# Performance work log

Hardware: AMD Instinct MI355X
Metric: run time of the kernel (lower is better)

## Reference

```python
import jax, jax.numpy as jnp
import numpy as np

# Module config (matches init_kwargs): inp_modes=[16,4,4,4], out_modes=[16,4,4,4], ranks=[1,8,8,1], 3x3 kernel
C_IN0, C_OUT0 = 16, 16          # leading conv channels
INP_MODES = (4, 4, 4)            # TT input modes -> c_inp = 64
OUT_MODES = (4, 4, 4)            # TT output modes -> c_out = 64
RANKS = (1, 8, 8, 1)
C_INP = int(np.prod(INP_MODES))  # 64
C_OUT = int(np.prod(OUT_MODES))  # 64


def setup_inputs() -> dict:
    key = jax.random.key(0)
    ks = jax.random.split(key, 5)
    x = jax.random.normal(ks[0], (8, C_IN0 * C_INP, 64, 64), jnp.float32)
    kernel = jax.random.normal(ks[1], (C_OUT0, C_IN0, 3, 3), jnp.float32) * (2.0 / (C_IN0 + C_OUT0))
    cores = {}
    for k in range(3):
        m, n = INP_MODES[k], OUT_MODES[k]
        cores[f"core{k}"] = jax.random.normal(ks[2 + k], (RANKS[k], m, n, RANKS[k + 1]), jnp.float32) * (2.0 / (m + n))
    b = jnp.ones((C_OUT,), jnp.float32)
    return {"x": x, "kernel": kernel, **cores, "b": b}


def _tt_matrix(core0, core1, core2):
    # Reconstruct W[(i1 i2 i3), (j1 j2 j3)] from TT cores (r_k, m_k, n_k, r_{k+1}).
    Wm = core0[0]  # (m1, n1, r1)  since r0 == 1
    for c in (core1, core2):
        Wm = jnp.einsum('...r,rmns->...mns', Wm, c)  # append (m_k, n_k) modes
    Wm = Wm[..., 0]  # drop trailing rank (== 1): (m1,n1,m2,n2,m3,n3)
    Wm = jnp.transpose(Wm, (0, 2, 4, 1, 3, 5))       # (m1,m2,m3,n1,n2,n3)
    return Wm.reshape(C_INP, C_OUT)


def reference(x, kernel, core0, core1, core2, b):
    B, Cin, H, W = x.shape  # Cin = C_IN0 * C_INP
    xr = x.reshape(-1, C_IN0, H, W)  # (B*c_inp, c_inp_0, H, W)
    y = jax.lax.conv_general_dilated(
        xr, kernel, window_strides=(1, 1), padding='VALID',
        dimension_numbers=('NCHW', 'OIHW', 'NCHW'))  # (B*c_inp, c_out_0, h, w)
    h, w = y.shape[-2], y.shape[-1]
    # Follow the torch reshape chain exactly
    y = y.reshape(B, C_INP, -1)                 # (B, c_inp, c_out_0*h*w)
    y = jnp.transpose(y, (0, 2, 1)).reshape(-1, C_INP)  # (B*c_out_0*h*w, c_inp)
    Wm = _tt_matrix(core0, core1, core2)        # (c_inp, c_out)
    out = y @ Wm + b                             # (B*c_out_0*h*w, c_out)
    return out.reshape(B, C_OUT0 * C_OUT, h, w)
```

## Files before the change

kernel.cpp:

```cpp
#include <hip/hip_runtime.h>
#include <hip/hip_bf16.h>

#define NB    8
#define NG    64
#define NCI   16
#define NC0   16
#define NJ    64
#define IH    64
#define IW    64
#define OH    62
#define OW    62
#define IPIX  4096
#define OPIX  3844

typedef __attribute__((ext_vector_type(8))) short  short8;
typedef __attribute__((ext_vector_type(4))) short  short4v;
typedef __attribute__((ext_vector_type(4))) float  float4v;

__device__ __forceinline__ unsigned short f2bf(float f) {
    unsigned int u = __builtin_bit_cast(unsigned int, f);
    unsigned int r = (u + 0x7fffu + ((u >> 16) & 1u)) >> 16;
    return (unsigned short)r;
}

__global__ __launch_bounds__(64) void prep_kernel(const float* __restrict__ K,
                                                  const float* __restrict__ c0_,
                                                  const float* __restrict__ c1_,
                                                  const float* __restrict__ c2_,
                                                  unsigned short* __restrict__ wmb,
                                                  unsigned short* __restrict__ kb) {
    int bi = blockIdx.x;
    int l  = threadIdx.x;
    if (bi < 8) {
        int jt = bi >> 1, kh = bi & 1;
        int j = jt * 16 + (l & 15);
        int j1 = j >> 4, j2 = (j >> 2) & 3, j3 = j & 3;
        for (int i = 0; i < 8; ++i) {
            int g = kh * 32 + (l >> 4) * 8 + i;
            int i1 = g >> 4, i2 = (g >> 2) & 3, i3 = g & 3;
            float s = 0.f;
            #pragma unroll
            for (int r1 = 0; r1 < 8; ++r1) {
                float a = c0_[(i1 * 4 + j1) * 8 + r1];
                float t = 0.f;
                #pragma unroll
                for (int r2 = 0; r2 < 8; ++r2) {
                    t += c1_[((r1 * 4 + i2) * 4 + j2) * 8 + r2] *
                         c2_[(r2 * 4 + i3) * 4 + j3];
                }
                s += a * t;
            }
            wmb[(bi * 64 + l) * 8 + i] = f2bf(s);
        }
    } else {
        int c0i = l & 15, q = l >> 4;
        for (int f = 0; f < 5; ++f) {
            int tap = f * 2 + (q >> 1);
            for (int i = 0; i < 8; ++i) {
                int ci = (q & 1) * 8 + i;
                float v = (tap < 9) ? K[(c0i * 16 + ci) * 9 + tap] : 0.f;
                kb[(f * 64 + l) * 8 + i] = f2bf(v);
            }
        }
    }
}

__global__ __launch_bounds__(256) void mix2_kernel(const float* __restrict__ x,
                                                   const unsigned short* __restrict__ wmb,
                                                   unsigned short* __restrict__ Z) {
    __shared__ __align__(16) char smem[32 * 2048];
    int t  = threadIdx.x;
    int b  = blockIdx.x >> 7;
    int p0 = (blockIdx.x & 127) * 32;

    int pq  = (t & 7) * 4;
    int grp = t >> 3;
    const float* xb = x + (size_t)b * 1024 * IPIX + p0 + pq;
    #pragma unroll 2
    for (int it = 0; it < 8; ++it) {
        int qd = it * 32 + grp;
        int gq = qd & 15, ci = qd >> 4;
        int g0 = gq * 4;
        const float* xp = xb + (size_t)(g0 * 16 + ci) * IPIX;
        float4v v0 = *(const float4v*)(xp);
        float4v v1 = *(const float4v*)(xp + 16 * IPIX);
        float4v v2 = *(const float4v*)(xp + 32 * IPIX);
        float4v v3 = *(const float4v*)(xp + 48 * IPIX);
        #pragma unroll
        for (int pp = 0; pp < 4; ++pp) {
            int px = pq + pp;
            short4v u;
            u[0] = (short)f2bf(v0[pp]);
            u[1] = (short)f2bf(v1[pp]);
            u[2] = (short)f2bf(v2[pp]);
            u[3] = (short)f2bf(v3[pp]);
            int chunk = (g0 >> 3) ^ (ci & 7) ^ (px & 7);
            *(short4v*)(smem + px * 2048 + ci * 128 + chunk * 16 + (g0 & 7) * 2) = u;
        }
    }
    __syncthreads();

    int lane = t & 63, wv = t >> 6;
    int ln = lane & 15, quad = lane >> 4;

    short8 bf[8];
    #pragma unroll
    for (int q8 = 0; q8 < 8; ++q8)
        bf[q8] = *(const short8*)(wmb + (q8 * 64 + lane) * 8);

    unsigned short* Zb = Z + (size_t)(b * IPIX + p0) * 1024;
    for (int k = 0; k < 8; ++k) {
        int pl = wv * 8 + k;
        const char* arow = smem + pl * 2048 + ln * 128;
        int sw = (ln & 7) ^ (pl & 7);
        short8 a0 = *(const short8*)(arow + (((0 + quad) ^ sw) * 16));
        short8 a1 = *(const short8*)(arow + (((4 + quad) ^ sw) * 16));
        unsigned short* zp = Zb + (size_t)pl * 1024 + ln * 16 + quad * 4;
        #pragma unroll
        for (int jt = 0; jt < 4; ++jt) {
            float4v acc = {0.f, 0.f, 0.f, 0.f};
            acc = __builtin_amdgcn_mfma_f32_16x16x32_bf16(a0, bf[jt * 2 + 0], acc, 0, 0, 0);
            acc = __builtin_amdgcn_mfma_f32_16x16x32_bf16(a1, bf[jt * 2 + 1], acc, 0, 0, 0);
            short4v o;
            o[0] = (short)f2bf(acc[0]); o[1] = (short)f2bf(acc[1]);
            o[2] = (short)f2bf(acc[2]); o[3] = (short)f2bf(acc[3]);
            *(short4v*)(zp + jt * 256) = o;
        }
    }
}

__global__ __launch_bounds__(256, 4) void conv2_kernel(const unsigned short* __restrict__ Z,
                                                       const unsigned short* __restrict__ kb,
                                                       const float* __restrict__ bias,
                                                       float* __restrict__ out) {
    int t = threadIdx.x, lane = t & 63, wv = t >> 6;
    int ln = lane & 15, quad = lane >> 4;
    int blk = blockIdx.x;
    int xh = blk & 1;
    int y  = (blk >> 1) % OH;
    int b  = blk / (OH * 2);

    short8 af[5];
    int off[5];
    #pragma unroll
    for (int f = 0; f < 5; ++f) {
        af[f] = *(const short8*)(kb + (f * 64 + lane) * 8);
        int tap = f * 2 + (quad >> 1);
        if (tap > 8) tap = 8;
        int dy = tap / 3, dx = tap % 3;
        off[f] = (dy * IW + dx) * 1024 + (wv * 16 + ln) * 16 + (quad & 1) * 8;
    }
    float4v bv = *(const float4v*)(bias + wv * 16 + quad * 4);

    const unsigned short* zbase = Z + (size_t)(b * IPIX + y * IW + xh * 31) * 1024;
    float* ob = out + ((size_t)(b * NC0 + ln) * OPIX + (size_t)(y * OW + xh * 31)) * NJ
                    + wv * 16 + quad * 4;

    #pragma unroll 2
    for (int xi = 0; xi < 31; ++xi) {
        const unsigned short* zp = zbase + (size_t)xi * 1024;
        short8 z0 = *(const short8*)(zp + off[0]);
        short8 z1 = *(const short8*)(zp + off[1]);
        short8 z2 = *(const short8*)(zp + off[2]);
        short8 z3 = *(const short8*)(zp + off[3]);
        short8 z4 = *(const short8*)(zp + off[4]);
        float4v acc = bv;
        acc = __builtin_amdgcn_mfma_f32_16x16x32_bf16(z0, af[0], acc, 0, 0, 0);
        acc = __builtin_amdgcn_mfma_f32_16x16x32_bf16(z1, af[1], acc, 0, 0, 0);
        acc = __builtin_amdgcn_mfma_f32_16x16x32_bf16(z2, af[2], acc, 0, 0, 0);
        acc = __builtin_amdgcn_mfma_f32_16x16x32_bf16(z3, af[3], acc, 0, 0, 0);
        acc = __builtin_amdgcn_mfma_f32_16x16x32_bf16(z4, af[4], acc, 0, 0, 0);
        *(float4v*)(ob + (size_t)xi * NJ) = acc;
    }
}

__global__ __launch_bounds__(64) void wm_kernel(const float* __restrict__ core0,
                                                const float* __restrict__ core1,
                                                const float* __restrict__ core2,
                                                float* __restrict__ Wm) {
    int g = threadIdx.x;
    int i1 = g >> 4, i2 = (g >> 2) & 3, i3 = g & 3;
    for (int j = 0; j < NJ; ++j) {
        int j1 = j >> 4, j2 = (j >> 2) & 3, j3 = j & 3;
        float s = 0.f;
        #pragma unroll
        for (int r1 = 0; r1 < 8; ++r1) {
            float a = core0[(i1 * 4 + j1) * 8 + r1];
            float t = 0.f;
            #pragma unroll
            for (int r2 = 0; r2 < 8; ++r2) {
                t += core1[((r1 * 4 + i2) * 4 + j2) * 8 + r2] *
                     core2[(r2 * 4 + i3) * 4 + j3];
            }
            s += a * t;
        }
        Wm[g * NJ + j] = s;
    }
}

__global__ __launch_bounds__(256) void fused_fallback(const float* __restrict__ x,
                                                      const float* __restrict__ K,
                                                      const float* __restrict__ Wm,
                                                      const float* __restrict__ bias,
                                                      float* __restrict__ out) {
    __shared__ float wlds[NG * NJ];
    __shared__ float klds[NCI * 9];
    int blk  = blockIdx.x;
    int pblk = blk & 15;
    int c0   = (blk >> 4) & 15;
    int b    = blk >> 8;
    for (int i = threadIdx.x; i < NG * NJ; i += 256) wlds[i] = Wm[i];
    for (int i = threadIdx.x; i < NCI * 9; i += 256) klds[i] = K[c0 * NCI * 9 + i];
    __syncthreads();

    int pix = pblk * 256 + threadIdx.x;
    if (pix >= OPIX) return;
    int y  = pix / OW;
    int xx = pix % OW;

    float acc[NJ];
    #pragma unroll
    for (int j = 0; j < NJ; ++j) acc[j] = 0.f;

    for (int g = 0; g < NG; ++g) {
        float c = 0.f;
        const float* xb = x + ((size_t)(b * NG + g) * NCI) * IPIX;
        for (int ci = 0; ci < NCI; ++ci) {
            #pragma unroll
            for (int dy = 0; dy < 3; ++dy) {
                #pragma unroll
                for (int dx = 0; dx < 3; ++dx) {
                    c += xb[ci * IPIX + (y + dy) * IW + (xx + dx)] *
                         klds[ci * 9 + dy * 3 + dx];
                }
            }
        }
        const float4* wp = (const float4*)&wlds[g * NJ];
        #pragma unroll
        for (int j4 = 0; j4 < 16; ++j4) {
            float4 w = wp[j4];
            acc[j4 * 4 + 0] += w.x * c;
            acc[j4 * 4 + 1] += w.y * c;
            acc[j4 * 4 + 2] += w.z * c;
            acc[j4 * 4 + 3] += w.w * c;
        }
    }
    #pragma unroll
    for (int j = 0; j < NJ; ++j) {
        out[(((size_t)(b * NC0 + c0) * OPIX) + pix) * NJ + j] = acc[j] + bias[j];
    }
}

extern "C" void kernel_launch(void* const* d_in, const int* in_sizes, int n_in,
                              void* d_out, int out_size, void* d_ws, size_t ws_size,
                              hipStream_t stream) {
    const float* x     = (const float*)d_in[0];
    const float* K     = (const float*)d_in[1];
    const float* core0 = (const float*)d_in[2];
    const float* core1 = (const float*)d_in[3];
    const float* core2 = (const float*)d_in[4];
    const float* bias  = (const float*)d_in[5];
    float* out = (float*)d_out;

    const size_t z_off   = 16384;
    const size_t z_bytes = (size_t)NB * IPIX * NJ * NCI * sizeof(unsigned short);

    if (ws_size >= z_off + z_bytes + 256) {
        unsigned short* wmb = (unsigned short*)d_ws;
        unsigned short* kb  = (unsigned short*)((char*)d_ws + 8192);
        unsigned short* Z   = (unsigned short*)((char*)d_ws + z_off);
        prep_kernel<<<9, 64, 0, stream>>>(K, core0, core1, core2, wmb, kb);
        mix2_kernel<<<NB * 128, 256, 0, stream>>>(x, wmb, Z);
        conv2_kernel<<<NB * OH * 2, 256, 0, stream>>>(Z, kb, bias, out);
    } else {
        float* Wm = (float*)d_ws;
        wm_kernel<<<1, 64, 0, stream>>>(core0, core1, core2, Wm);
        fused_fallback<<<NB * NC0 * 16, 256, 0, stream>>>(x, K, Wm, bias, out);
    }
}
```

Before: 113.4 us.

## Split mixing into separate transpose-to-bf16 pass and LDS-free MFMA mix kernel

Moves the fp32-to-bf16 conversion and channel-major to pixel-major transpose of x out of the mix kernel into a dedicated transpose kernel that writes a bf16 intermediate buffer. The mix kernel then reads contiguous bf16 rows directly from global memory with no shared-memory staging. The aim is better-coalesced reads of x in longer runs per row. In exchange it adds a full extra write and read of a 64 MB bf16 intermediate and needs twice the workspace, which may send execution to the fallback path if the workspace is too small.

```diff
diff --git a/kernel.cpp b/kernel.cpp
--- a/kernel.cpp
+++ b/kernel.cpp
@@ -65,42 +65,45 @@
     }
 }
 
-__global__ __launch_bounds__(256) void mix2_kernel(const float* __restrict__ x,
+__global__ __launch_bounds__(256) void xt_kernel(const float* __restrict__ x,
+                                                 unsigned short* __restrict__ xf) {
+    __shared__ unsigned short lds[256 * 128];
+    int t    = threadIdx.x;
+    int bi   = blockIdx.x;
+    int pxb  = bi & 15;
+    int coct = (bi >> 4) & 7;
+    int b    = bi >> 7;
+    int px0  = pxb * 256;
+    int wv = t >> 6, l = t & 63;
+
+    const float* xb = x + ((size_t)(b * 1024 + coct * 128) * IPIX) + px0 + 4 * l;
+    int swz = (l & 15) << 3;
+    #pragma unroll 4
+    for (int s = 0; s < 32; ++s) {
+        int r = wv * 32 + s;
+        float4v v = *(const float4v*)(xb + (size_t)r * IPIX);
+        int pc  = (r & 15) * 8 + (r >> 4);
+        int pcs = pc ^ swz;
+        #pragma unroll
+        for (int p = 0; p < 4; ++p) {
+            lds[(4 * l + p) * 128 + pcs] = f2bf(v[p]);
+        }
+    }
+    __syncthreads();
+
+    int lo = t & 15, ph = t >> 4;
+    unsigned short* ob = xf + ((size_t)(b * IPIX + px0) * 1024) + coct * 128 + lo * 8;
+    for (int w = 0; w < 16; ++w) {
+        int px = w * 16 + ph;
+        short8 v = *(const short8*)(lds + px * 128 + ((lo ^ ((px >> 2) & 15)) * 8));
+        *(short8*)(ob + (size_t)px * 1024) = v;
+    }
+}
+
+__global__ __launch_bounds__(256) void mixf_kernel(const unsigned short* __restrict__ xf,
                                                    const unsigned short* __restrict__ wmb,
                                                    unsigned short* __restrict__ Z) {
-    __shared__ __align__(16) char smem[32 * 2048];
-    int t  = threadIdx.x;
-    int b  = blockIdx.x >> 7;
-    int p0 = (blockIdx.x & 127) * 32;
-
-    int pq  = (t & 7) * 4;
-    int grp = t >> 3;
-    const float* xb = x + (size_t)b * 1024 * IPIX + p0 + pq;
-    #pragma unroll 2
-    for (int it = 0; it < 8; ++it) {
-        int qd = it * 32 + grp;
-        int gq = qd & 15, ci = qd >> 4;
-        int g0 = gq * 4;
-        const float* xp = xb + (size_t)(g0 * 16 + ci) * IPIX;
-        float4v v0 = *(const float4v*)(xp);
-        float4v v1 = *(const float4v*)(xp + 16 * IPIX);
-        float4v v2 = *(const float4v*)(xp + 32 * IPIX);
-        float4v v3 = *(const float4v*)(xp + 48 * IPIX);
-        #pragma unroll
-        for (int pp = 0; pp < 4; ++pp) {
-            int px = pq + pp;
-            short4v u;
-            u[0] = (short)f2bf(v0[pp]);
-            u[1] = (short)f2bf(v1[pp]);
-            u[2] = (short)f2bf(v2[pp]);
-            u[3] = (short)f2bf(v3[pp]);
-            int chunk = (g0 >> 3) ^ (ci & 7) ^ (px & 7);
-            *(short4v*)(smem + px * 2048 + ci * 128 + chunk * 16 + (g0 & 7) * 2) = u;
-        }
-    }
-    __syncthreads();
-
-    int lane = t & 63, wv = t >> 6;
+    int t = threadIdx.x, lane = t & 63, wv = t >> 6;
     int ln = lane & 15, quad = lane >> 4;
 
     short8 bf[8];
@@ -108,14 +111,15 @@
     for (int q8 = 0; q8 < 8; ++q8)
         bf[q8] = *(const short8*)(wmb + (q8 * 64 + lane) * 8);
 
-    unsigned short* Zb = Z + (size_t)(b * IPIX + p0) * 1024;
-    for (int k = 0; k < 8; ++k) {
-        int pl = wv * 8 + k;
-        const char* arow = smem + pl * 2048 + ln * 128;
-        int sw = (ln & 7) ^ (pl & 7);
-        short8 a0 = *(const short8*)(arow + (((0 + quad) ^ sw) * 16));
-        short8 a1 = *(const short8*)(arow + (((4 + quad) ^ sw) * 16));
-        unsigned short* zp = Zb + (size_t)pl * 1024 + ln * 16 + quad * 4;
+    int P0 = blockIdx.x * 32 + wv * 8;
+    const unsigned short* xr = xf + (size_t)P0 * 1024 + quad * 128 + ln * 8;
+    unsigned short* zr = Z + (size_t)P0 * 1024 + ln * 16 + quad * 4;
+
+    #pragma unroll 2
+    for (int i = 0; i < 8; ++i) {
+        short8 a0 = *(const short8*)(xr + (size_t)i * 1024);
+        short8 a1 = *(const short8*)(xr + (size_t)i * 1024 + 512);
+        unsigned short* zp = zr + (size_t)i * 1024;
         #pragma unroll
         for (int jt = 0; jt < 4; ++jt) {
             float4v acc = {0.f, 0.f, 0.f, 0.f};
@@ -265,12 +269,14 @@
     const size_t z_off   = 16384;
     const size_t z_bytes = (size_t)NB * IPIX * NJ * NCI * sizeof(unsigned short);
 
-    if (ws_size >= z_off + z_bytes + 256) {
+    if (ws_size >= z_off + 2 * z_bytes + 256) {
         unsigned short* wmb = (unsigned short*)d_ws;
         unsigned short* kb  = (unsigned short*)((char*)d_ws + 8192);
-        unsigned short* Z   = (unsigned short*)((char*)d_ws + z_off);
+        unsigned short* xf  = (unsigned short*)((char*)d_ws + z_off);
+        unsigned short* Z   = (unsigned short*)((char*)d_ws + z_off + z_bytes);
         prep_kernel<<<9, 64, 0, stream>>>(K, core0, core1, core2, wmb, kb);
-        mix2_kernel<<<NB * 128, 256, 0, stream>>>(x, wmb, Z);
+        xt_kernel<<<1024, 256, 0, stream>>>(x, xf);
+        mixf_kernel<<<1024, 256, 0, stream>>>(xf, wmb, Z);
         conv2_kernel<<<NB * OH * 2, 256, 0, stream>>>(Z, kb, bias, out);
     } else {
         float* Wm = (float*)d_ws;
```

Result: slower. 136.1 us (+20.0%).
